# Optimization experiments

Hardware: AMD Instinct MI355X
Metric: run time of the kernel (lower is better)

The kernel has to match this reference:

```python
import jax, jax.numpy as jnp
import numpy as np

D = 64       # CNF state dimension
H = 512      # MLP hidden width
B = 8192     # batch


def setup_inputs() -> dict:
    key = jax.random.key(0)
    ks = jax.random.split(key, 8)
    s1 = 1.0 / np.sqrt(D + 1)
    s2 = 1.0 / np.sqrt(H)
    return {
        "t": jax.random.uniform(ks[0], (1,), dtype=jnp.float32),
        "x": jax.random.normal(ks[1], (B, D + 1), dtype=jnp.float32),
        "W1": jax.random.normal(ks[2], (D + 1, H), dtype=jnp.float32) * s1,
        "b1": jnp.zeros((H,), dtype=jnp.float32),
        "W2": jax.random.normal(ks[3], (H, H), dtype=jnp.float32) * s2,
        "b2": jnp.zeros((H,), dtype=jnp.float32),
        "W3": jax.random.normal(ks[4], (H, D), dtype=jnp.float32) * s2,
        "b3": jnp.zeros((D,), dtype=jnp.float32),
    }


def reference(t, x, W1, b1, W2, b2, W3, b3):
    # CNF.forward: strip log-density channel, evaluate vf and its exact divergence.
    xs = x[..., :-1]                      # [B, D]
    tt = t[0]

    def vf_single(xi):                    # xi: [D] -> [D]
        inp = jnp.concatenate([tt[None], xi])          # vf(t*ones, x) with t prepended
        h = jnp.tanh(inp @ W1 + b1)
        h = jnp.tanh(h @ W2 + b2)
        return h @ W3 + b3

    dx = jax.vmap(vf_single)(xs)                        # [B, D]
    # exact divergence: trace of per-sample Jacobian via reverse-mode (matches torch jacrev)
    J = jax.vmap(jax.jacrev(vf_single))(xs)             # [B, D, D]
    div = jnp.trace(J, axis1=-2, axis2=-1)              # [B]
    return jnp.concatenate([dx, div[:, None]], axis=-1) # [B, D+1]
```

## Files before the change

kernel.cpp:

```cpp
#include <hip/hip_runtime.h>

#define HH 512
#define DD 64
#define MROWS 32
#define TPB 1024
#define LP 520

typedef unsigned short u16;
typedef short s16x8 __attribute__((ext_vector_type(8)));
typedef float f32x4 __attribute__((ext_vector_type(4)));

#define MFMA16(A,B,C) __builtin_amdgcn_mfma_f32_16x16x32_bf16((A),(B),(C),0,0,0)

#define OFF_W2K  0
#define OFF_EFK  262144
#define OFF_W1F  524288
#define OFF_W3F  557056
#define OFF_Z0B  (589824 * 2)

__device__ __forceinline__ u16 f2bf(float f) {
    unsigned u = __builtin_bit_cast(unsigned, f);
    u += 0x7fffu + ((u >> 16) & 1u);
    return (u16)(u >> 16);
}
__device__ __forceinline__ float bf2f(u16 h) {
    return __builtin_bit_cast(float, (unsigned)h << 16);
}
__device__ __forceinline__ float fast_tanh(float x) {
    float e = __expf(2.0f * x);
    return 1.0f - 2.0f * __builtin_amdgcn_rcpf(e + 1.0f);
}

__device__ __forceinline__ void stage2(const u16* gbase, int chunk, u16* sbuf,
                                       int w, int lane) {
#pragma unroll
    for (int r = 0; r < 2; ++r) {
        const u16* g = gbase + chunk * 16384 + (2 * w + r) * 512 + lane * 8;
        u16* l = sbuf + (2 * w + r) * 512;
        __builtin_amdgcn_global_load_lds(
            (const __attribute__((address_space(1))) unsigned int*)g,
            (__attribute__((address_space(3))) unsigned int*)l, 16, 0, 0);
    }
}

__global__ __launch_bounds__(256) void precompute(
    const float* __restrict__ t,  const float* __restrict__ W1,
    const float* __restrict__ b1, const float* __restrict__ W2,
    const float* __restrict__ W3, u16* __restrict__ ws16, float* __restrict__ z0)
{
    __shared__ float T[16 * 264 > 256 * 20 ? 16 * 264 : 256 * 20];
    u16* W2K = ws16 + OFF_W2K;
    u16* EFK = ws16 + OFF_EFK;
    u16* W1F = ws16 + OFF_W1F;
    u16* W3F = ws16 + OFF_W3F;

    const int bid = blockIdx.x, tid = threadIdx.x;
    const int lane = tid & 63, wv = tid >> 6;
    const int m16 = lane & 15, q = lane >> 4;

    if (bid < 64) {
        const int nt = bid >> 1, bh = bid & 1;
        const int a0 = nt * 16, b0 = bh * 256;
        s16x8 afh[2], afl[2];
#pragma unroll
        for (int h = 0; h < 2; ++h)
#pragma unroll
            for (int j = 0; j < 8; ++j) {
                int i = h * 32 + q * 8 + j;
                float v = W1[(1 + i) * HH + a0 + m16];
                u16 hi = f2bf(v);
                afh[h][j] = (short)hi;
                afl[h][j] = (short)f2bf(v - bf2f(hi));
            }
#pragma unroll
        for (int bt = 0; bt < 4; ++bt) {
            int bl = wv * 64 + bt * 16;
            s16x8 bfh[2], bfl[2];
#pragma unroll
            for (int h = 0; h < 2; ++h) {
                const float* src = W3 + (b0 + bl + m16) * DD + h * 32 + q * 8;
                float4 p0 = *(const float4*)(src);
                float4 p1 = *(const float4*)(src + 4);
                float vv[8] = {p0.x,p0.y,p0.z,p0.w,p1.x,p1.y,p1.z,p1.w};
#pragma unroll
                for (int j = 0; j < 8; ++j) {
                    u16 hi = f2bf(vv[j]);
                    bfh[h][j] = (short)hi;
                    bfl[h][j] = (short)f2bf(vv[j] - bf2f(hi));
                }
            }
            f32x4 c = {0.f, 0.f, 0.f, 0.f};
#pragma unroll
            for (int h = 0; h < 2; ++h) {
                c = MFMA16(afh[h], bfh[h], c);
                c = MFMA16(afh[h], bfl[h], c);
                c = MFMA16(afl[h], bfh[h], c);
            }
#pragma unroll
            for (int r = 0; r < 4; ++r)
                T[(4 * q + r) * 264 + bl + m16] = c[r];
        }
        __syncthreads();
#pragma unroll
        for (int p = 0; p < 2; ++p) {
            int ksl = p * 4 + wv;
            int al  = m16;
            int blc = ksl * 32 + q * 8;
            const float* w2p = W2 + (a0 + al) * HH + b0 + blc;
            float4 wa = *(const float4*)(w2p), wb = *(const float4*)(w2p + 4);
            const float* glp = T + al * 264 + blc;
            s16x8 o;
            o[0]=(short)f2bf(wa.x*glp[0]); o[1]=(short)f2bf(wa.y*glp[1]);
            o[2]=(short)f2bf(wa.z*glp[2]); o[3]=(short)f2bf(wa.w*glp[3]);
            o[4]=(short)f2bf(wb.x*glp[4]); o[5]=(short)f2bf(wb.y*glp[5]);
            o[6]=(short)f2bf(wb.z*glp[6]); o[7]=(short)f2bf(wb.w*glp[7]);
            *(s16x8*)(EFK + (b0 / 32 + ksl) * 16384 + nt * 512 + lane * 8) = o;
        }
        if (bh == 0 && tid < 128) {
            int ks = tid >> 6, ln = tid & 63;
            int n  = nt * 16 + (ln & 15);
            int k0 = ks * 32 + (ln >> 4) * 8;
            s16x8 o;
#pragma unroll
            for (int j = 0; j < 8; ++j) o[j] = (short)f2bf(W1[(1 + k0 + j) * HH + n]);
            *(s16x8*)(W1F + nt * 1024 + ks * 512 + ln * 8) = o;
        }
    } else if (bid < 128) {
        const int nt = (bid - 64) >> 1, kh = (bid - 64) & 1;
        const int n0 = nt * 16, k0 = kh * 256;
#pragma unroll
        for (int it = 0; it < 4; ++it) {
            int r = (tid >> 2) + it * 64;
            int c = (tid & 3) * 4;
            float4 v = *(const float4*)(W2 + (k0 + r) * HH + n0 + c);
            *(float4*)(T + r * 20 + c) = v;
        }
        __syncthreads();
#pragma unroll
        for (int p = 0; p < 2; ++p) {
            int ksl = p * 4 + wv;
            int kqx = ksl * 32 + q * 8;
            s16x8 o;
#pragma unroll
            for (int j = 0; j < 8; ++j) o[j] = (short)f2bf(T[(kqx + j) * 20 + m16]);
            *(s16x8*)(W2K + (k0 / 32 + ksl) * 16384 + nt * 512 + lane * 8) = o;
        }
    } else if (bid < 136) {
        const int ot = (bid - 128) >> 1, kh = (bid - 128) & 1;
        const int o0 = ot * 16, k0 = kh * 256;
#pragma unroll
        for (int it = 0; it < 4; ++it) {
            int r = (tid >> 2) + it * 64;
            int c = (tid & 3) * 4;
            float4 v = *(const float4*)(W3 + (k0 + r) * DD + o0 + c);
            *(float4*)(T + r * 20 + c) = v;
        }
        __syncthreads();
#pragma unroll
        for (int p = 0; p < 2; ++p) {
            int ksl = p * 4 + wv;
            int kqx = ksl * 32 + q * 8;
            s16x8 o;
#pragma unroll
            for (int j = 0; j < 8; ++j) o[j] = (short)f2bf(T[(kqx + j) * 20 + m16]);
            *(s16x8*)(W3F + ot * 8192 + (k0 / 32 + ksl) * 512 + lane * 8) = o;
        }
    } else {
        for (int n = tid; n < HH; n += 256)
            z0[n] = b1[n] + t[0] * W1[n];
    }
}

__global__ __launch_bounds__(TPB) void cnf_main(
    const float* __restrict__ x,  const u16* __restrict__ ws16,
    const float* __restrict__ z0, const float* __restrict__ b2,
    const float* __restrict__ b3, float* __restrict__ out)
{
    __shared__ u16 h1s[MROWS * LP];
    __shared__ u16 h2s[MROWS * LP];
    __shared__ u16 stg[2][16384];
    __shared__ float z0s[HH];
    __shared__ float b2s[HH];
    __shared__ float b3s[DD];
    __shared__ float divacc[16][MROWS];

    const u16* W2K = ws16 + OFF_W2K;
    const u16* EFK = ws16 + OFF_EFK;
    const u16* W1F = ws16 + OFF_W1F;
    const u16* W3F = ws16 + OFF_W3F;

    const int tid  = threadIdx.x;
    const int lane = tid & 63;
    const int w    = tid >> 6;
    const int m16  = lane & 15;
    const int q    = lane >> 4;
    const int kq   = q * 8;
    const int r0   = blockIdx.x * MROWS;
    const int col0 = 2 * w * 16 + m16;
    const int col1 = (2 * w + 1) * 16 + m16;

    u16* xs = stg[1];

    stage2(W2K, 0, stg[0], w, lane);

    for (int idx = tid; idx < MROWS * DD; idx += TPB) {
        int r = idx >> 6, c = idx & 63;
        xs[r * 72 + c] = f2bf(x[(r0 + r) * (DD + 1) + c]);
    }
    if (tid < HH) { z0s[tid] = z0[tid]; b2s[tid] = b2[tid]; }
    if (tid < DD) b3s[tid] = b3[tid];

    s16x8 p1b[2][2];
#pragma unroll
    for (int ct = 0; ct < 2; ++ct) {
        const u16* bb = W1F + (2 * w + ct) * 1024 + lane * 8;
        p1b[ct][0] = *(const s16x8*)(bb);
        p1b[ct][1] = *(const s16x8*)(bb + 512);
    }
    __syncthreads();

    float d1reg[2][2][4];

    {
        s16x8 xa[2][2];
#pragma unroll
        for (int rt = 0; rt < 2; ++rt)
#pragma unroll
            for (int h = 0; h < 2; ++h)
                xa[rt][h] = *(const s16x8*)(xs + (rt * 16 + m16) * 72 + h * 32 + kq);
#pragma unroll
        for (int ct = 0; ct < 2; ++ct) {
            int col = ct ? col1 : col0;
#pragma unroll
            for (int rt = 0; rt < 2; ++rt) {
                f32x4 c = {0.f, 0.f, 0.f, 0.f};
                c = MFMA16(xa[rt][0], p1b[ct][0], c);
                c = MFMA16(xa[rt][1], p1b[ct][1], c);
#pragma unroll
                for (int i = 0; i < 4; ++i) {
                    float hv = fast_tanh(c[i] + z0s[col]);
                    h1s[(rt * 16 + 4 * q + i) * LP + col] = f2bf(hv);
                    d1reg[rt][ct][i] = 1.0f - hv * hv;
                }
            }
        }
    }

    f32x4 a00={0,0,0,0}, a01={0,0,0,0}, a10={0,0,0,0}, a11={0,0,0,0};
#pragma unroll
    for (int ks = 0; ks < 16; ++ks) {
        __syncthreads();
        if (ks < 15) stage2(W2K, ks + 1, stg[(ks + 1) & 1], w, lane);
        const u16* sb = stg[ks & 1];
        s16x8 b0 = *(const s16x8*)(sb + (2 * w) * 512 + lane * 8);
        s16x8 b1v = *(const s16x8*)(sb + (2 * w + 1) * 512 + lane * 8);
        s16x8 f0 = *(const s16x8*)(h1s + m16 * LP + ks * 32 + kq);
        s16x8 f1 = *(const s16x8*)(h1s + (16 + m16) * LP + ks * 32 + kq);
        a00 = MFMA16(f0, b0, a00);
        a10 = MFMA16(f1, b0, a10);
        a01 = MFMA16(f0, b1v, a01);
        a11 = MFMA16(f1, b1v, a11);
    }

    {
        f32x4 acc[2][2] = {{a00, a01}, {a10, a11}};
#pragma unroll
        for (int rt = 0; rt < 2; ++rt)
#pragma unroll
            for (int ct = 0; ct < 2; ++ct) {
                int col = ct ? col1 : col0;
#pragma unroll
                for (int i = 0; i < 4; ++i)
                    h2s[(rt * 16 + 4 * q + i) * LP + col] =
                        f2bf(fast_tanh(acc[rt][ct][i] + b2s[col]));
            }
    }
    __syncthreads();

    stage2(EFK, 0, stg[0], w, lane);

    if (w < 8) {
        const int rowt = w >> 2, ot = w & 3;
        const u16* ap = h2s + (rowt * 16 + m16) * LP + kq;
        const u16* bp = W3F + ot * 8192 + lane * 8;
        s16x8 W3r[4];
#pragma unroll
        for (int k = 0; k < 4; ++k) W3r[k] = *(const s16x8*)(bp + k * 512);
        f32x4 cA = {0.f,0.f,0.f,0.f}, cB = {0.f,0.f,0.f,0.f};
#pragma unroll
        for (int ks = 0; ks < 16; ++ks) {
            s16x8 f = *(const s16x8*)(ap + ks * 32);
            const int sl = ks & 3;
            if (ks & 1) cB = MFMA16(f, W3r[sl], cB);
            else        cA = MFMA16(f, W3r[sl], cA);
            if (ks < 12) W3r[sl] = *(const s16x8*)(bp + (ks + 4) * 512);
        }
        f32x4 c3 = cA + cB;
        int o = ot * 16 + m16;
#pragma unroll
        for (int i = 0; i < 4; ++i)
            out[(r0 + rowt * 16 + 4 * q + i) * (DD + 1) + o] = c3[i] + b3s[o];
    }
    __syncthreads();

#pragma unroll
    for (int p = 0; p < 2; ++p) {
        int g = tid + p * TPB;
        int row = g >> 6, colv = (g & 63) * 8;
        u16* pp = h2s + row * LP + colv;
        s16x8 hv = *(const s16x8*)pp;
        s16x8 dv;
#pragma unroll
        for (int j = 0; j < 8; ++j) {
            float f = bf2f((u16)hv[j]);
            dv[j] = (short)f2bf(1.0f - f * f);
        }
        *(s16x8*)pp = dv;
    }

    {
        f32x4 g00={0,0,0,0}, g01={0,0,0,0}, g10={0,0,0,0}, g11={0,0,0,0};
#pragma unroll
        for (int ks = 0; ks < 16; ++ks) {
            __syncthreads();
            if (ks < 15) stage2(EFK, ks + 1, stg[(ks + 1) & 1], w, lane);
            const u16* sb = stg[ks & 1];
            s16x8 e0 = *(const s16x8*)(sb + (2 * w) * 512 + lane * 8);
            s16x8 e1 = *(const s16x8*)(sb + (2 * w + 1) * 512 + lane * 8);
            s16x8 f0 = *(const s16x8*)(h2s + m16 * LP + ks * 32 + kq);
            s16x8 f1 = *(const s16x8*)(h2s + (16 + m16) * LP + ks * 32 + kq);
            g00 = MFMA16(f0, e0, g00);
            g10 = MFMA16(f1, e0, g10);
            g01 = MFMA16(f0, e1, g01);
            g11 = MFMA16(f1, e1, g11);
        }
        f32x4 acc[2][2] = {{g00, g01}, {g10, g11}};
#pragma unroll
        for (int rt = 0; rt < 2; ++rt)
#pragma unroll
            for (int i = 0; i < 4; ++i) {
                float v = d1reg[rt][0][i] * acc[rt][0][i]
                        + d1reg[rt][1][i] * acc[rt][1][i];
                v += __shfl_xor(v, 1, 64);
                v += __shfl_xor(v, 2, 64);
                v += __shfl_xor(v, 4, 64);
                v += __shfl_xor(v, 8, 64);
                if (m16 == 0) divacc[w][rt * 16 + 4 * q + i] = v;
            }
    }
    __syncthreads();

    if (tid < MROWS) {
        float s = 0.0f;
#pragma unroll
        for (int ww = 0; ww < 16; ++ww) s += divacc[ww][tid];
        out[(r0 + tid) * (DD + 1) + DD] = s;
    }
}

extern "C" void kernel_launch(void* const* d_in, const int* in_sizes, int n_in,
                              void* d_out, int out_size, void* d_ws, size_t ws_size,
                              hipStream_t stream) {
    const float* t  = (const float*)d_in[0];
    const float* x  = (const float*)d_in[1];
    const float* W1 = (const float*)d_in[2];
    const float* b1 = (const float*)d_in[3];
    const float* W2 = (const float*)d_in[4];
    const float* b2 = (const float*)d_in[5];
    const float* W3 = (const float*)d_in[6];
    const float* b3 = (const float*)d_in[7];
    float* out = (float*)d_out;

    u16*   ws16 = (u16*)d_ws;
    float* z0   = (float*)((char*)d_ws + OFF_Z0B);

    precompute<<<137, 256, 0, stream>>>(t, W1, b1, W2, W3, ws16, z0);
    cnf_main<<<8192 / MROWS, TPB, 0, stream>>>(x, ws16, z0, b2, b3, out);
}
```

Before: 102.3 us.

## Shrink blocks to 16 rows with per-wave private async weight staging

Result: no change. 104.3 us (+1.9%).

```diff
diff --git a/kernel.cpp b/kernel.cpp
--- a/kernel.cpp
+++ b/kernel.cpp
@@ -2,8 +2,8 @@
 
 #define HH 512
 #define DD 64
-#define MROWS 32
-#define TPB 1024
+#define MROWS 16
+#define TPB 256
 #define LP 520
 
 typedef unsigned short u16;
@@ -30,17 +30,19 @@
     float e = __expf(2.0f * x);
     return 1.0f - 2.0f * __builtin_amdgcn_rcpf(e + 1.0f);
 }
-
-__device__ __forceinline__ void stage2(const u16* gbase, int chunk, u16* sbuf,
-                                       int w, int lane) {
-#pragma unroll
-    for (int r = 0; r < 2; ++r) {
-        const u16* g = gbase + chunk * 16384 + (2 * w + r) * 512 + lane * 8;
-        u16* l = sbuf + (2 * w + r) * 512;
-        __builtin_amdgcn_global_load_lds(
-            (const __attribute__((address_space(1))) unsigned int*)g,
-            (__attribute__((address_space(3))) unsigned int*)l, 16, 0, 0);
-    }
+__device__ __forceinline__ void gll(const u16* g, u16* l) {
+    __builtin_amdgcn_global_load_lds(
+        (const __attribute__((address_space(1))) unsigned int*)g,
+        (__attribute__((address_space(3))) unsigned int*)l, 16, 0, 0);
+}
+__device__ __forceinline__ void wait_vm4() {
+    asm volatile("s_waitcnt vmcnt(4)" ::: "memory");
+}
+__device__ __forceinline__ void wait_vm0() {
+    asm volatile("s_waitcnt vmcnt(0)" ::: "memory");
+}
+__device__ __forceinline__ void fence_lds_reads() {
+    asm volatile("s_waitcnt lgkmcnt(0)" ::: "memory");
 }
 
 __global__ __launch_bounds__(256) void precompute(
@@ -178,11 +180,11 @@
 {
     __shared__ u16 h1s[MROWS * LP];
     __shared__ u16 h2s[MROWS * LP];
-    __shared__ u16 stg[2][16384];
+    __shared__ u16 stg[2][8192];
     __shared__ float z0s[HH];
     __shared__ float b2s[HH];
     __shared__ float b3s[DD];
-    __shared__ float divacc[16][MROWS];
+    __shared__ float divacc[4][MROWS];
 
     const u16* W2K = ws16 + OFF_W2K;
     const u16* EFK = ws16 + OFF_EFK;
@@ -196,164 +198,175 @@
     const int q    = lane >> 4;
     const int kq   = q * 8;
     const int r0   = blockIdx.x * MROWS;
-    const int col0 = 2 * w * 16 + m16;
-    const int col1 = (2 * w + 1) * 16 + m16;
-
-    u16* xs = stg[1];
-
-    stage2(W2K, 0, stg[0], w, lane);
+
+    u16* xs = h2s;
 
     for (int idx = tid; idx < MROWS * DD; idx += TPB) {
         int r = idx >> 6, c = idx & 63;
         xs[r * 72 + c] = f2bf(x[(r0 + r) * (DD + 1) + c]);
     }
-    if (tid < HH) { z0s[tid] = z0[tid]; b2s[tid] = b2[tid]; }
+    for (int n = tid; n < HH; n += TPB) { z0s[n] = z0[n]; b2s[n] = b2[n]; }
     if (tid < DD) b3s[tid] = b3[tid];
 
-    s16x8 p1b[2][2];
-#pragma unroll
-    for (int ct = 0; ct < 2; ++ct) {
-        const u16* bb = W1F + (2 * w + ct) * 1024 + lane * 8;
-        p1b[ct][0] = *(const s16x8*)(bb);
-        p1b[ct][1] = *(const s16x8*)(bb + 512);
+    s16x8 b1f[8][2];
+#pragma unroll
+    for (int j = 0; j < 8; ++j) {
+        const u16* bb = W1F + (w * 8 + j) * 1024 + lane * 8;
+        b1f[j][0] = *(const s16x8*)(bb);
+        b1f[j][1] = *(const s16x8*)(bb + 512);
     }
     __syncthreads();
 
-    float d1reg[2][2][4];
-
     {
-        s16x8 xa[2][2];
-#pragma unroll
-        for (int rt = 0; rt < 2; ++rt)
-#pragma unroll
-            for (int h = 0; h < 2; ++h)
-                xa[rt][h] = *(const s16x8*)(xs + (rt * 16 + m16) * 72 + h * 32 + kq);
-#pragma unroll
-        for (int ct = 0; ct < 2; ++ct) {
-            int col = ct ? col1 : col0;
-#pragma unroll
-            for (int rt = 0; rt < 2; ++rt) {
-                f32x4 c = {0.f, 0.f, 0.f, 0.f};
-                c = MFMA16(xa[rt][0], p1b[ct][0], c);
-                c = MFMA16(xa[rt][1], p1b[ct][1], c);
-#pragma unroll
-                for (int i = 0; i < 4; ++i) {
-                    float hv = fast_tanh(c[i] + z0s[col]);
-                    h1s[(rt * 16 + 4 * q + i) * LP + col] = f2bf(hv);
-                    d1reg[rt][ct][i] = 1.0f - hv * hv;
-                }
-            }
-        }
-    }
-
-    f32x4 a00={0,0,0,0}, a01={0,0,0,0}, a10={0,0,0,0}, a11={0,0,0,0};
-#pragma unroll
-    for (int ks = 0; ks < 16; ++ks) {
-        __syncthreads();
-        if (ks < 15) stage2(W2K, ks + 1, stg[(ks + 1) & 1], w, lane);
-        const u16* sb = stg[ks & 1];
-        s16x8 b0 = *(const s16x8*)(sb + (2 * w) * 512 + lane * 8);
-        s16x8 b1v = *(const s16x8*)(sb + (2 * w + 1) * 512 + lane * 8);
-        s16x8 f0 = *(const s16x8*)(h1s + m16 * LP + ks * 32 + kq);
-        s16x8 f1 = *(const s16x8*)(h1s + (16 + m16) * LP + ks * 32 + kq);
-        a00 = MFMA16(f0, b0, a00);
-        a10 = MFMA16(f1, b0, a10);
-        a01 = MFMA16(f0, b1v, a01);
-        a11 = MFMA16(f1, b1v, a11);
-    }
+        s16x8 xa0 = *(const s16x8*)(xs + m16 * 72 + kq);
+        s16x8 xa1 = *(const s16x8*)(xs + m16 * 72 + 32 + kq);
+#pragma unroll
+        for (int j = 0; j < 8; ++j) {
+            f32x4 c = {0.f, 0.f, 0.f, 0.f};
+            c = MFMA16(xa0, b1f[j][0], c);
+            c = MFMA16(xa1, b1f[j][1], c);
+            int col = (w * 8 + j) * 16 + m16;
+#pragma unroll
+            for (int i = 0; i < 4; ++i)
+                h1s[(4 * q + i) * LP + col] = f2bf(fast_tanh(c[i] + z0s[col]));
+        }
+    }
+    __syncthreads();
 
     {
-        f32x4 acc[2][2] = {{a00, a01}, {a10, a11}};
-#pragma unroll
-        for (int rt = 0; rt < 2; ++rt)
-#pragma unroll
-            for (int ct = 0; ct < 2; ++ct) {
-                int col = ct ? col1 : col0;
+        const u16* abase = h1s + m16 * LP + kq;
+        u16* my0 = stg[0] + w * 2048;
+        u16* my1 = stg[1] + w * 2048;
+#pragma unroll
+        for (int g = 0; g < 2; ++g) {
+            const u16* wbase = W2K + (g * 16 + w * 4) * 512 + lane * 8;
+            fence_lds_reads();
+#pragma unroll
+            for (int j = 0; j < 4; ++j) gll(wbase + j * 512,         my0 + j * 512);
+#pragma unroll
+            for (int j = 0; j < 4; ++j) gll(wbase + 16384 + j * 512, my1 + j * 512);
+            f32x4 acc[4];
+#pragma unroll
+            for (int j = 0; j < 4; ++j) acc[j] = f32x4{0.f,0.f,0.f,0.f};
+#pragma unroll 4
+            for (int c = 0; c < 16; ++c) {
+                if (c < 15) wait_vm4(); else wait_vm0();
+                u16* sb = (c & 1) ? my1 : my0;
+                s16x8 bf0 = *(const s16x8*)(sb +        lane * 8);
+                s16x8 bf1 = *(const s16x8*)(sb +  512 + lane * 8);
+                s16x8 bf2 = *(const s16x8*)(sb + 1024 + lane * 8);
+                s16x8 bf3 = *(const s16x8*)(sb + 1536 + lane * 8);
+                s16x8 af  = *(const s16x8*)(abase + c * 32);
+                acc[0] = MFMA16(af, bf0, acc[0]);
+                acc[1] = MFMA16(af, bf1, acc[1]);
+                acc[2] = MFMA16(af, bf2, acc[2]);
+                acc[3] = MFMA16(af, bf3, acc[3]);
+                if (c < 14) {
+                    fence_lds_reads();
+                    const u16* src = wbase + (c + 2) * 16384;
+#pragma unroll
+                    for (int j = 0; j < 4; ++j) gll(src + j * 512, sb + j * 512);
+                }
+            }
+#pragma unroll
+            for (int j = 0; j < 4; ++j) {
+                int col = (g * 16 + w * 4 + j) * 16 + m16;
 #pragma unroll
                 for (int i = 0; i < 4; ++i)
-                    h2s[(rt * 16 + 4 * q + i) * LP + col] =
-                        f2bf(fast_tanh(acc[rt][ct][i] + b2s[col]));
-            }
+                    h2s[(4 * q + i) * LP + col] = f2bf(fast_tanh(acc[j][i] + b2s[col]));
+            }
+        }
     }
     __syncthreads();
 
-    stage2(EFK, 0, stg[0], w, lane);
-
-    if (w < 8) {
-        const int rowt = w >> 2, ot = w & 3;
-        const u16* ap = h2s + (rowt * 16 + m16) * LP + kq;
-        const u16* bp = W3F + ot * 8192 + lane * 8;
+    {
+        const u16* ap = h2s + m16 * LP + kq;
+        const u16* bp = W3F + w * 8192 + lane * 8;
         s16x8 W3r[4];
 #pragma unroll
         for (int k = 0; k < 4; ++k) W3r[k] = *(const s16x8*)(bp + k * 512);
         f32x4 cA = {0.f,0.f,0.f,0.f}, cB = {0.f,0.f,0.f,0.f};
 #pragma unroll
-        for (int ks = 0; ks < 16; ++ks) {
-            s16x8 f = *(const s16x8*)(ap + ks * 32);
-            const int sl = ks & 3;
-            if (ks & 1) cB = MFMA16(f, W3r[sl], cB);
-            else        cA = MFMA16(f, W3r[sl], cA);
-            if (ks < 12) W3r[sl] = *(const s16x8*)(bp + (ks + 4) * 512);
+        for (int c = 0; c < 16; ++c) {
+            s16x8 f = *(const s16x8*)(ap + c * 32);
+            const int sl = c & 3;
+            if (c & 1) cB = MFMA16(f, W3r[sl], cB);
+            else       cA = MFMA16(f, W3r[sl], cA);
+            if (c < 12) W3r[sl] = *(const s16x8*)(bp + (c + 4) * 512);
         }
         f32x4 c3 = cA + cB;
-        int o = ot * 16 + m16;
+        int o = w * 16 + m16;
 #pragma unroll
         for (int i = 0; i < 4; ++i)
-            out[(r0 + rowt * 16 + 4 * q + i) * (DD + 1) + o] = c3[i] + b3s[o];
+            out[(r0 + 4 * q + i) * (DD + 1) + o] = c3[i] + b3s[o];
+    }
+
+    {
+        const u16* abase = h2s + m16 * LP + kq;
+        u16* my0 = stg[0] + w * 2048;
+        u16* my1 = stg[1] + w * 2048;
+        float dpart[4] = {0.f, 0.f, 0.f, 0.f};
+#pragma unroll
+        for (int g = 0; g < 2; ++g) {
+            const u16* ebase = EFK + (g * 16 + w * 4) * 512 + lane * 8;
+            fence_lds_reads();
+#pragma unroll
+            for (int j = 0; j < 4; ++j) gll(ebase + j * 512,         my0 + j * 512);
+#pragma unroll
+            for (int j = 0; j < 4; ++j) gll(ebase + 16384 + j * 512, my1 + j * 512);
+            f32x4 acc[4];
+#pragma unroll
+            for (int j = 0; j < 4; ++j) acc[j] = f32x4{0.f,0.f,0.f,0.f};
+#pragma unroll 4
+            for (int c = 0; c < 16; ++c) {
+                if (c < 15) wait_vm4(); else wait_vm0();
+                u16* sb = (c & 1) ? my1 : my0;
+                s16x8 bf0 = *(const s16x8*)(sb +        lane * 8);
+                s16x8 bf1 = *(const s16x8*)(sb +  512 + lane * 8);
+                s16x8 bf2 = *(const s16x8*)(sb + 1024 + lane * 8);
+                s16x8 bf3 = *(const s16x8*)(sb + 1536 + lane * 8);
+                s16x8 hf  = *(const s16x8*)(abase + c * 32);
+                s16x8 af;
+#pragma unroll
+                for (int jj = 0; jj < 8; ++jj) {
+                    float f = bf2f((u16)hf[jj]);
+                    af[jj] = (short)f2bf(1.0f - f * f);
+                }
+                acc[0] = MFMA16(af, bf0, acc[0]);
+                acc[1] = MFMA16(af, bf1, acc[1]);
+                acc[2] = MFMA16(af, bf2, acc[2]);
+                acc[3] = MFMA16(af, bf3, acc[3]);
+                if (c < 14) {
+                    fence_lds_reads();
+                    const u16* src = ebase + (c + 2) * 16384;
+#pragma unroll
+                    for (int j = 0; j < 4; ++j) gll(src + j * 512, sb + j * 512);
+                }
+            }
+#pragma unroll
+            for (int j = 0; j < 4; ++j) {
+                int col = (g * 16 + w * 4 + j) * 16 + m16;
+#pragma unroll
+                for (int i = 0; i < 4; ++i) {
+                    float h1v = bf2f(h1s[(4 * q + i) * LP + col]);
+                    dpart[i] += (1.0f - h1v * h1v) * acc[j][i];
+                }
+            }
+        }
+#pragma unroll
+        for (int i = 0; i < 4; ++i) {
+            float v = dpart[i];
+            v += __shfl_xor(v, 1, 64);
+            v += __shfl_xor(v, 2, 64);
+            v += __shfl_xor(v, 4, 64);
+            v += __shfl_xor(v, 8, 64);
+            if (m16 == 0) divacc[w][4 * q + i] = v;
+        }
     }
     __syncthreads();
 
-#pragma unroll
-    for (int p = 0; p < 2; ++p) {
-        int g = tid + p * TPB;
-        int row = g >> 6, colv = (g & 63) * 8;
-        u16* pp = h2s + row * LP + colv;
-        s16x8 hv = *(const s16x8*)pp;
-        s16x8 dv;
-#pragma unroll
-        for (int j = 0; j < 8; ++j) {
-            float f = bf2f((u16)hv[j]);
-            dv[j] = (short)f2bf(1.0f - f * f);
-        }
-        *(s16x8*)pp = dv;
-    }
-
-    {
-        f32x4 g00={0,0,0,0}, g01={0,0,0,0}, g10={0,0,0,0}, g11={0,0,0,0};
-#pragma unroll
-        for (int ks = 0; ks < 16; ++ks) {
-            __syncthreads();
-            if (ks < 15) stage2(EFK, ks + 1, stg[(ks + 1) & 1], w, lane);
-            const u16* sb = stg[ks & 1];
-            s16x8 e0 = *(const s16x8*)(sb + (2 * w) * 512 + lane * 8);
-            s16x8 e1 = *(const s16x8*)(sb + (2 * w + 1) * 512 + lane * 8);
-            s16x8 f0 = *(const s16x8*)(h2s + m16 * LP + ks * 32 + kq);
-            s16x8 f1 = *(const s16x8*)(h2s + (16 + m16) * LP + ks * 32 + kq);
-            g00 = MFMA16(f0, e0, g00);
-            g10 = MFMA16(f1, e0, g10);
-            g01 = MFMA16(f0, e1, g01);
-            g11 = MFMA16(f1, e1, g11);
-        }
-        f32x4 acc[2][2] = {{g00, g01}, {g10, g11}};
-#pragma unroll
-        for (int rt = 0; rt < 2; ++rt)
-#pragma unroll
-            for (int i = 0; i < 4; ++i) {
-                float v = d1reg[rt][0][i] * acc[rt][0][i]
-                        + d1reg[rt][1][i] * acc[rt][1][i];
-                v += __shfl_xor(v, 1, 64);
-                v += __shfl_xor(v, 2, 64);
-                v += __shfl_xor(v, 4, 64);
-                v += __shfl_xor(v, 8, 64);
-                if (m16 == 0) divacc[w][rt * 16 + 4 * q + i] = v;
-            }
-    }
-    __syncthreads();
-
     if (tid < MROWS) {
-        float s = 0.0f;
-#pragma unroll
-        for (int ww = 0; ww < 16; ++ww) s += divacc[ww][tid];
+        float s = divacc[0][tid] + divacc[1][tid] + divacc[2][tid] + divacc[3][tid];
         out[(r0 + tid) * (DD + 1) + DD] = s;
     }
 }
```
